# Kernel optimization log

Hardware: AMD Instinct MI355X
Metric: run time of the kernel (lower is better)

The kernel has to match this reference:

```python
import jax, jax.numpy as jnp
import numpy as np

N = 2048   # num nodes
D = 512    # hidden_dim


def setup_inputs() -> dict:
    key = jax.random.key(0)
    k1, k2 = jax.random.split(key)
    x = jax.random.normal(k1, (N, D), dtype=jnp.float32)
    # linear: hidden_dim -> 1 (xavier-like scale)
    w = jax.random.normal(k2, (D,), dtype=jnp.float32) * (1.0 / np.sqrt(D))
    b = jnp.zeros((1,), dtype=jnp.float32)
    return {"x": x, "w": w, "b": b}


def reference(x, w, b):
    # euclidean_distance_matrix + linear fused:
    # s[i,j] = sum_d w_d * (x[i,d]-x[j,d])^2 + b
    #        = q_i + q_j - 2*(x*w) @ x^T + b,  q_i = sum_d w_d x[i,d]^2
    xw = x * w                              # [N, D]
    q = jnp.sum(xw * x, axis=1)             # [N]
    cross = xw @ x.T                        # [N, N]
    s = q[:, None] + q[None, :] - 2.0 * cross + b[0]
    grouping_matrix = jax.nn.sigmoid(s)     # [N, N]

    # compute_fielder, similarity_graph='base'
    W = grouping_matrix
    degree = jnp.sum(W, axis=1)
    L = jnp.diag(degree) - W                # symmetric graph Laplacian
    eigen_values, eigen_vectors = jnp.linalg.eigh(L)
    order = jnp.argsort(jnp.abs(eigen_values))
    fielder_value = eigen_values[order[1]]
    fielder_vector = eigen_vectors[:, order[1]]
    return grouping_matrix, fielder_value, fielder_vector
```

## Files before the change

### kernel.cpp

```cpp
#include <hip/hip_runtime.h>
#include <math.h>

constexpr int NN = 2048;
constexpr int DD_ = 512;
constexpr int LM = 64;
constexpr int VS = NN + 32;
constexpr int GPART = 8;
#define SIGN_FLIP 1


typedef __attribute__((ext_vector_type(4))) float f32x4;
typedef __attribute__((ext_vector_type(8))) short bf16x8;

__device__ inline double waveReduceSum(double v) {
#pragma unroll
  for (int off = 32; off; off >>= 1) v += __shfl_down(v, off, 64);
  return v;
}

__device__ inline double blockReduceSum256(double v) {
  __shared__ double sm[4];
  int lane = threadIdx.x & 63;
  int wid  = threadIdx.x >> 6;
  v = waveReduceSum(v);
  __syncthreads();
  if (lane == 0) sm[wid] = v;
  __syncthreads();
  double r = 0.0;
  if (threadIdx.x < 4) r = sm[threadIdx.x];
  if (wid == 0) {
    r += __shfl_down(r, 2, 64);
    r += __shfl_down(r, 1, 64);
  }
  return r;
}

__device__ inline double blockReduceSum128(double v) {
  __shared__ double sm[2];
  int lane = threadIdx.x & 63;
  int wid  = threadIdx.x >> 6;
  v = waveReduceSum(v);
  if (lane == 0) sm[wid] = v;
  __syncthreads();
  double r = 0.0;
  if (threadIdx.x == 0) r = sm[0] + sm[1];
  return r;
}

__device__ inline unsigned short f2bf(float f) {
  unsigned u = __float_as_uint(f);
  u += 0x7FFFu + ((u >> 16) & 1u);
  return (unsigned short)(u >> 16);
}
__device__ inline float bf2f(unsigned short h) {
  return __uint_as_float(((unsigned)h) << 16);
}

__global__ __launch_bounds__(128) void k_cvtq(const float* __restrict__ x,
                                              const float* __restrict__ w,
                                              float* __restrict__ q,
                                              unsigned short* __restrict__ ah,
                                              unsigned short* __restrict__ al,
                                              unsigned short* __restrict__ bh,
                                              unsigned short* __restrict__ bl) {
  int row = blockIdx.x, t = threadIdx.x;
  int d = 4 * t;
  float4 xv = *(const float4*)&x[(size_t)row * DD_ + d];
  float4 wv = *(const float4*)&w[d];
  float xs[4] = {xv.x, xv.y, xv.z, xv.w};
  float wsv[4] = {wv.x, wv.y, wv.z, wv.w};
  unsigned short rah[4], ral[4], rbh[4], rbl[4];
  float accq = 0.f;
#pragma unroll
  for (int kq = 0; kq < 4; ++kq) {
    float xf = xs[kq], wf = wsv[kq];
    float a = xf * wf;
    unsigned short h = f2bf(a);
    rah[kq] = h;
    ral[kq] = f2bf(a - bf2f(h));
    unsigned short hb = f2bf(xf);
    rbh[kq] = hb;
    rbl[kq] = f2bf(xf - bf2f(hb));
    accq += wf * xf * xf;
  }
  ushort4 vA = {rah[0], rah[1], rah[2], rah[3]};
  ushort4 vAl = {ral[0], ral[1], ral[2], ral[3]};
  ushort4 vB = {rbh[0], rbh[1], rbh[2], rbh[3]};
  ushort4 vBl = {rbl[0], rbl[1], rbl[2], rbl[3]};
  *(ushort4*)&ah[(size_t)row * DD_ + d] = vA;
  *(ushort4*)&al[(size_t)row * DD_ + d] = vAl;
  *(ushort4*)&bh[(size_t)row * DD_ + d] = vB;
  *(ushort4*)&bl[(size_t)row * DD_ + d] = vBl;
  double rq = blockReduceSum128((double)accq);
  if (t == 0) q[row] = (float)rq;
}

__global__ __launch_bounds__(256) void k_Wm(const unsigned short* __restrict__ ah,
                                            const unsigned short* __restrict__ al,
                                            const unsigned short* __restrict__ bh,
                                            const unsigned short* __restrict__ bl,
                                            const float* __restrict__ q,
                                            const float* __restrict__ bptr,
                                            float* __restrict__ out) {
  const int bx = blockIdx.x, by = blockIdx.y;
  if (bx < by) return;
  __shared__ unsigned short As[2][128][40];
  __shared__ unsigned short Bs[2][128][40];
  const int t = threadIdx.x;
  const int i0 = by * 128, j0 = bx * 128;
  const int lane = t & 63, wv = t >> 6;
  const int wr = wv >> 1, wc = wv & 1;
  const int fr = lane & 15, kc = lane >> 4;
  const int srow = t >> 1, scol = (t & 1) * 16;

  f32x4 acc[4][4];
#pragma unroll
  for (int a = 0; a < 4; ++a)
#pragma unroll
    for (int b = 0; b < 4; ++b) acc[a][b] = (f32x4){0.f, 0.f, 0.f, 0.f};

  {
    bf16x8 ra0 = *(const bf16x8*)&ah[(size_t)(i0 + srow) * DD_ + scol];
    bf16x8 ra1 = *(const bf16x8*)&ah[(size_t)(i0 + srow) * DD_ + scol + 8];
    bf16x8 rb0 = *(const bf16x8*)&bh[(size_t)(j0 + srow) * DD_ + scol];
    bf16x8 rb1 = *(const bf16x8*)&bh[(size_t)(j0 + srow) * DD_ + scol + 8];
    *(bf16x8*)&As[0][srow][scol] = ra0;
    *(bf16x8*)&As[0][srow][scol + 8] = ra1;
    *(bf16x8*)&Bs[0][srow][scol] = rb0;
    *(bf16x8*)&Bs[0][srow][scol + 8] = rb1;
  }
  __syncthreads();
  int cur = 0;
  for (int s = 0; s < 48; ++s) {
    bf16x8 na0, na1, nb0, nb1;
    if (s + 1 < 48) {
      int pass = (s + 1) >> 4;
      int kk = ((s + 1) & 15) * 32;
      const unsigned short* srcA = (pass == 2) ? al : ah;
      const unsigned short* srcB = (pass == 1) ? bl : bh;
      na0 = *(const bf16x8*)&srcA[(size_t)(i0 + srow) * DD_ + kk + scol];
      na1 = *(const bf16x8*)&srcA[(size_t)(i0 + srow) * DD_ + kk + scol + 8];
      nb0 = *(const bf16x8*)&srcB[(size_t)(j0 + srow) * DD_ + kk + scol];
      nb1 = *(const bf16x8*)&srcB[(size_t)(j0 + srow) * DD_ + kk + scol + 8];
    }
    bf16x8 af[4], bq[4];
#pragma unroll
    for (int a = 0; a < 4; ++a)
      af[a] = *(const bf16x8*)&As[cur][wr * 64 + a * 16 + fr][kc * 8];
#pragma unroll
    for (int b = 0; b < 4; ++b)
      bq[b] = *(const bf16x8*)&Bs[cur][wc * 64 + b * 16 + fr][kc * 8];
#pragma unroll
    for (int a = 0; a < 4; ++a)
#pragma unroll
      for (int b = 0; b < 4; ++b)
        acc[a][b] = __builtin_amdgcn_mfma_f32_16x16x32_bf16(af[a], bq[b], acc[a][b], 0, 0, 0);
    if (s + 1 < 48) {
      *(bf16x8*)&As[cur ^ 1][srow][scol] = na0;
      *(bf16x8*)&As[cur ^ 1][srow][scol + 8] = na1;
      *(bf16x8*)&Bs[cur ^ 1][srow][scol] = nb0;
      *(bf16x8*)&Bs[cur ^ 1][srow][scol + 8] = nb1;
    }
    __syncthreads();
    cur ^= 1;
  }
  float b0 = bptr[0];
  const bool mirror = (bx != by);
#pragma unroll
  for (int a = 0; a < 4; ++a) {
#pragma unroll
    for (int rg = 0; rg < 4; ++rg) {
      int i = i0 + wr * 64 + a * 16 + kc * 4 + rg;
      float qi = q[i];
#pragma unroll
      for (int b = 0; b < 4; ++b) {
        int j = j0 + wc * 64 + b * 16 + fr;
        float s = qi + q[j] - 2.0f * acc[a][b][rg] + b0;
        float sig = 1.0f / (1.0f + expf(-s));
        out[(size_t)i * NN + j] = sig;
        if (mirror) out[(size_t)j * NN + i] = sig;
      }
    }
  }
}

__global__ __launch_bounds__(256) void k_init(double* __restrict__ r,
                                              double* __restrict__ part) {
  int t = threadIdx.x;
  double loc[8];
  double s = 0.0;
#pragma unroll
  for (int p = 0; p < 8; ++p) {
    unsigned i = (unsigned)(t + 256 * p);
    unsigned u = i * 2654435761u + 0x9E3779B9u;
    u ^= u >> 16; u *= 0x85EBCA6Bu; u ^= u >> 13; u *= 0xC2B2AE35u; u ^= u >> 16;
    double val = ((double)u / 4294967296.0) - 0.5;
    loc[p] = val; s += val;
  }
  __shared__ double mean_s, inv_s;
  double tot = blockReduceSum256(s);
  if (t == 0) mean_s = tot / (double)NN;
  __syncthreads();
  double mean = mean_s;
  double ss = 0.0;
#pragma unroll
  for (int p = 0; p < 8; ++p) { loc[p] -= mean; ss += loc[p] * loc[p]; }
  double tss = blockReduceSum256(ss);
  if (t == 0) inv_s = 1.0 / sqrt(tss);
  __syncthreads();
  double inv = inv_s;
#pragma unroll
  for (int p = 0; p < 8; ++p) r[t + 256 * p] = loc[p] * inv;
  if (t < GPART) part[t] = (t == 0) ? 1.0 : 0.0;
}

__global__ __launch_bounds__(256) void k_mva(const float* __restrict__ Wm,
                                             double* __restrict__ deg,
                                             const double* __restrict__ rprev,
                                             const double* __restrict__ part,
                                             double* __restrict__ V,
                                             double* __restrict__ wstash,
                                             double* __restrict__ c,
                                             double* __restrict__ beta, int j) {
  int b = blockIdx.x, t = threadIdx.x;
  double ss = 0.0;
#pragma unroll
  for (int p = 0; p < GPART; ++p) ss += part[p];
  double bet = sqrt(ss);
  double inv = (bet > 1e-3) ? 1.0 / bet : 0.0;

  if (b < NN) {
    const float* wr = Wm + (size_t)b * NN;
    double acc = 0.0, dsum = 0.0;
    if (j == 0) {
#pragma unroll
      for (int p = 0; p < 2; ++p) {
        int i = 4 * t + 1024 * p;
        float4 wl = *(const float4*)&wr[i];
        dsum += (double)wl.x + (double)wl.y + (double)wl.z + (double)wl.w;
        acc += (double)wl.x * rprev[i] + (double)wl.y * rprev[i + 1] +
               (double)wl.z * rprev[i + 2] + (double)wl.w * rprev[i + 3];
      }
    } else {
#pragma unroll
      for (int p = 0; p < 2; ++p) {
        int i = 4 * t + 1024 * p;
        float4 wl = *(const float4*)&wr[i];
        acc += (double)wl.x * rprev[i] + (double)wl.y * rprev[i + 1] +
               (double)wl.z * rprev[i + 2] + (double)wl.w * rprev[i + 3];
      }
    }
    double red = blockReduceSum256(acc);
    double dred = 0.0;
    if (j == 0) dred = blockReduceSum256(dsum);
    if (t == 0) {
      double d;
      if (j == 0) { d = dred; deg[b] = d; }
      else d = deg[b];
      double vj = rprev[b] * inv;
      V[(size_t)j * VS + b] = vj;
      wstash[(size_t)j * VS + b] = d * vj - red * inv;
      if (b == 0 && j > 0) beta[j - 1] = (bet > 1e-3) ? bet : 0.0;
    }
  } else {
    int q = b - NN;
    const double* wq = wstash + (size_t)q * VS;
    double a = 0.0;
#pragma unroll
    for (int p = 0; p < 8; ++p) { int i = t + 256 * p; a += wq[i] * rprev[i]; }
    double red = blockReduceSum256(a);
    if (t == 0) c[q] = red * inv;
  }
}

__global__ __launch_bounds__(256) void k_orthb(const double* __restrict__ V,
                                               const double* __restrict__ wstash,
                                               const double* __restrict__ c,
                                               double* __restrict__ r,
                                               double* __restrict__ part,
                                               double* __restrict__ alpha, int j) {
  __shared__ double cs[LM];
  __shared__ double cj_s, s1_s;
  int b = blockIdx.x, t = threadIdx.x;
  const double* wj = wstash + (size_t)j * VS;
  const double* vj = V + (size_t)j * VS;
  double a = 0.0, s = 0.0;
#pragma unroll
  for (int p = 0; p < 8; ++p) {
    int i = t + 256 * p;
    double wv = wj[i];
    a += vj[i] * wv;
    s += wv;
  }
  double cj = blockReduceSum256(a);
  double s1 = blockReduceSum256(s);
  if (t == 0) { cj_s = cj; s1_s = s1; }
  for (int k = t; k < j; k += 256) cs[k] = c[k];
  __syncthreads();
  double cjv = cj_s, s1v = s1_s;
  int i = b * 256 + t;
  double val = wj[i] - s1v / (double)NN - cjv * vj[i];
  for (int k = 0; k < j; ++k) val -= cs[k] * V[(size_t)k * VS + i];
  r[i] = val;
  double rr = blockReduceSum256(val * val);
  if (t == 0) {
    part[b] = rr;
    if (b == 0) alpha[j] = cjv;
  }
}

__device__ inline double guardpiv(double d) {
  if (fabs(d) < 1e-280) return (d < 0.0) ? -1e-280 : 1e-280;
  return d;
}

__global__ __launch_bounds__(64) void k_tri(const double* __restrict__ alpha,
                                            const double* __restrict__ beta,
                                            double* __restrict__ svec) {
  const int t = threadIdx.x;
  double al_r = alpha[t];
  double be_r = (t < LM - 1) ? beta[t] : 0.0;

  int cand = isfinite(al_r) ? LM : t;
  int candb = (t < LM - 1 && (be_r == 0.0 || !isfinite(be_r))) ? (t + 1) : LM;
  int m = min(cand, candb);
#pragma unroll
  for (int off = 32; off; off >>= 1) m = min(m, __shfl_down(m, off, 64));
  m = __shfl(m, 0, 64);
  if (m < 2) m = 2;
  const int n = m;

  double be_prev = __shfl_up(be_r, 1, 64);
  double lo = 1e300, hi = -1e300;
  if (t < n) {
    double rr = 0.0;
    if (t > 0) rr += fabs(be_prev);
    if (t < n - 1) rr += fabs(be_r);
    lo = al_r - rr;
    hi = al_r + rr;
  }
#pragma unroll
  for (int off = 32; off; off >>= 1) {
    lo = fmin(lo, __shfl_down(lo, off, 64));
    hi = fmax(hi, __shfl_down(hi, off, 64));
  }
  lo = __shfl(lo, 0, 64);
  hi = __shfl(hi, 0, 64);

  double B0 = lo, B1 = hi;
  for (int round = 0; round < 3; ++round) {
    double p = B0 + (B1 - B0) * ((double)(t + 1) / 65.0);
    int cnt = 0;
    double d = __shfl(al_r, 0, 64) - p;
    if (d < 0) cnt++;
    for (int i = 1; i < n; ++i) {
      double ai = __shfl(al_r, i, 64);
      double bi = __shfl(be_r, i - 1, 64);
      if (fabs(d) < 1e-300) d = (d < 0.0) ? -1e-300 : 1e-300;
      d = (ai - p) - bi * bi / d;
      if (d < 0) cnt++;
    }
    unsigned long long nz = __ballot(cnt > 0);
    double nl, nh;
    if (nz) {
      int first = __ffsll(nz) - 1;
      nh = B0 + (B1 - B0) * ((double)(first + 1) / 65.0);
      nl = (first > 0) ? (B0 + (B1 - B0) * ((double)first / 65.0)) : B0;
    } else {
      nl = B0 + (B1 - B0) * (64.0 / 65.0);
      nh = B1;
    }
    B0 = nl; B1 = nh;
  }
  const double sigma = 0.5 * (B0 + B1);

  double Dgf = 0.0, Dl_s = 0.0, Du_s = 0.0, Du2_s = 0.0;
  int piv_s = 0;
  {
    double dg = __shfl(al_r, 0, 64) - sigma;
    double du = __shfl(be_r, 0, 64);
    for (int i = 0; i < n - 1; ++i) {
      double bl = __shfl(be_r, i, 64);
      double a_ip1 = __shfl(al_r, i + 1, 64);
      double be_ip1 = (i + 1 < n - 1) ? __shfl(be_r, i + 1, 64) : 0.0;
      double dg_ip1 = a_ip1 - sigma;
      double dg_n, du_n;
      if (fabs(dg) >= fabs(bl)) {
        double fact = bl / guardpiv(dg);
        if (t == i) { Dgf = dg; Dl_s = fact; Du_s = du; Du2_s = 0.0; piv_s = 0; }
        dg_n = dg_ip1 - fact * du;
        du_n = be_ip1;
      } else {
        double fact = dg / bl;
        if (t == i) { Dgf = bl; Dl_s = fact; Du_s = dg_ip1; Du2_s = be_ip1; piv_s = 1; }
        dg_n = du - fact * dg_ip1;
        du_n = -fact * be_ip1;
      }
      dg = dg_n; du = du_n;
    }
    if (t == n - 1) Dgf = dg;
  }

  double bbf = 1.0;
  {
    double cur = 1.0;
    for (int i = 0; i < n - 1; ++i) {
      double dl = __shfl(Dl_s, i, 64);
      int pv = __shfl(piv_s, i, 64);
      double nxt;
      if (!pv) {
        if (t == i) bbf = cur;
        nxt = 1.0 - dl * cur;
      } else {
        if (t == i) bbf = 1.0;
        nxt = cur - dl;
      }
      cur = nxt;
    }
    if (t == n - 1) bbf = cur;
  }

  double xv = 0.0;
  {
    double x_ip1 = 0.0, x_ip2 = 0.0;
    for (int i = n - 1; i >= 0; --i) {
      double bi = __shfl(bbf, i, 64);
      double dgi = __shfl(Dgf, i, 64);
      double dui = __shfl(Du_s, i, 64);
      double du2i = __shfl(Du2_s, i, 64);
      double num = bi;
      if (i < n - 1) num -= dui * x_ip1;
      if (i < n - 2) num -= du2i * x_ip2;
      double xi = num / guardpiv(dgi);
      if (t == i) xv = xi;
      x_ip2 = x_ip1; x_ip1 = xi;
    }
  }

  double nrm = (t < n) ? xv * xv : 0.0;
#pragma unroll
  for (int off = 32; off; off >>= 1) nrm += __shfl_down(nrm, off, 64);
  nrm = __shfl(nrm, 0, 64);
  double s = 1.0 / sqrt(nrm);
  svec[t] = (t < n) ? xv * s : 0.0;
}

__global__ __launch_bounds__(256) void k_ritz(const double* __restrict__ V,
                                              const double* __restrict__ s,
                                              double* __restrict__ u) {
  __shared__ double cs[LM];
  int t = threadIdx.x;
  for (int k = t; k < LM; k += 256) cs[k] = s[k];
  __syncthreads();
  int i = blockIdx.x * 256 + t;
  double acc = 0.0;
  for (int k = 0; k < LM; ++k) acc += cs[k] * V[(size_t)k * VS + i];
  u[i] = acc;
}

__global__ __launch_bounds__(256) void k_mvu(const float* __restrict__ Wm,
                                             const double* __restrict__ deg,
                                             const double* __restrict__ v,
                                             double* __restrict__ w) {
  int row = blockIdx.x, t = threadIdx.x;
  const float* wr = Wm + (size_t)row * NN;
  double acc = 0.0;
#pragma unroll
  for (int p = 0; p < 2; ++p) {
    int i = 4 * t + 1024 * p;
    float4 wl = *(const float4*)&wr[i];
    acc += (double)wl.x * v[i] + (double)wl.y * v[i + 1] +
           (double)wl.z * v[i + 2] + (double)wl.w * v[i + 3];
  }
  double r = blockReduceSum256(acc);
  if (t == 0) w[row] = deg[row] * v[row] - r;
}

__global__ __launch_bounds__(256) void k_tail(const double* __restrict__ u,
                                              const double* __restrict__ lu,
                                              float* __restrict__ out_lam,
                                              float* __restrict__ outv) {
  __shared__ double mv[256];
  __shared__ int mi[256];
  __shared__ double mean_s, scale_s;
  int t = threadIdx.x;
  double a = 0.0, b = 0.0;
#pragma unroll
  for (int p = 0; p < 8; ++p) {
    int i = t + 256 * p;
    a += u[i] * lu[i];
    b += u[i] * u[i];
  }
  double ra = blockReduceSum256(a);
  double rb = blockReduceSum256(b);
  if (t == 0) *out_lam = (float)(ra / rb);
  double loc[8];
  double s = 0.0;
#pragma unroll
  for (int p = 0; p < 8; ++p) { loc[p] = u[t + 256 * p]; s += loc[p]; }
  double tot = blockReduceSum256(s);
  if (t == 0) mean_s = tot / (double)NN;
  __syncthreads();
  double mean = mean_s;
  double ss = 0.0, bv = -1.0;
  int bi = 0;
#pragma unroll
  for (int p = 0; p < 8; ++p) {
    loc[p] -= mean;
    ss += loc[p] * loc[p];
    double aa = fabs(loc[p]);
    if (aa > bv) { bv = aa; bi = p; }
  }
  double tss = blockReduceSum256(ss);
  mv[t] = bv; mi[t] = t + 256 * bi;
  __syncthreads();
  for (int off = 128; off; off >>= 1) {
    if (t < off) {
      if (mv[t + off] > mv[t]) { mv[t] = mv[t + off]; mi[t] = mi[t + off]; }
    }
    __syncthreads();
  }
  if (t == 0) {
    int gi = mi[0];
    double best = u[gi] - mean_s;
    double sgn = (best < 0.0) ? -1.0 : 1.0;
#if SIGN_FLIP
    sgn = -sgn;
#endif
    scale_s = sgn / sqrt(tss);
  }
  __syncthreads();
  double sc = scale_s;
#pragma unroll
  for (int p = 0; p < 8; ++p) outv[t + 256 * p] = (float)(loc[p] * sc);
}

extern "C" void kernel_launch(void* const* d_in, const int* in_sizes, int n_in,
                              void* d_out, int out_size, void* d_ws, size_t ws_size,
                              hipStream_t stream) {
  const float* x = (const float*)d_in[0];
  const float* wv = (const float*)d_in[1];
  const float* bp = (const float*)d_in[2];
  float* out = (float*)d_out;

  char* ws = (char*)d_ws;
  size_t off = 0;
  auto alloc = [&](size_t bytes) -> char* {
    char* p = ws + off;
    off = (off + bytes + 255) & ~(size_t)255;
    return p;
  };
  float* q      = (float*)alloc((size_t)NN * 4);
  double* deg   = (double*)alloc((size_t)NN * 8);
  double* r     = (double*)alloc((size_t)NN * 8);
  double* u     = (double*)alloc((size_t)NN * 8);
  double* c     = (double*)alloc((size_t)(LM + 2) * 8);
  double* alpha = (double*)alloc((size_t)LM * 8);
  double* beta  = (double*)alloc((size_t)LM * 8);
  double* svec  = (double*)alloc((size_t)LM * 8);
  double* part  = (double*)alloc((size_t)GPART * 8);
  char* un = alloc((size_t)4 * NN * DD_ * 2);
  unsigned short* ah = (unsigned short*)un;
  unsigned short* al = ah + (size_t)NN * DD_;
  unsigned short* bh = al + (size_t)NN * DD_;
  unsigned short* bl = bh + (size_t)NN * DD_;
  double* V      = (double*)un;
  double* wstash = V + (size_t)LM * VS;
  (void)ws_size; (void)in_sizes; (void)n_in; (void)out_size;

  k_cvtq<<<NN, 128, 0, stream>>>(x, wv, q, ah, al, bh, bl);
  dim3 g(NN / 128, NN / 128);
  k_Wm<<<g, 256, 0, stream>>>(ah, al, bh, bl, q, bp, out);
  k_init<<<1, 256, 0, stream>>>(r, part);

  for (int j = 0; j < LM; ++j) {
    k_mva<<<NN + j, 256, 0, stream>>>(out, deg, r, part, V, wstash, c, beta, j);
    k_orthb<<<NN / 256, 256, 0, stream>>>(V, wstash, c, r, part, alpha, j);
  }
  k_tri<<<1, 64, 0, stream>>>(alpha, beta, svec);
  k_ritz<<<NN / 256, 256, 0, stream>>>(V, svec, u);
  k_mvu<<<NN, 256, 0, stream>>>(out, deg, u, r);
  k_tail<<<1, 256, 0, stream>>>(u, r, out + (size_t)NN * NN,
                                out + (size_t)NN * NN + 1);
}
```

Baseline: 825.0 us.

## Coalesce mirrored sigmoid writes via LDS transpose and prefetch shuffles in tridiagonal solve

The GEMM epilogue used to write the mirrored (transposed) tile with scattered, column-strided stores. It now keeps the sigmoid values in the accumulators, transposes them through a shared-memory buffer unioned with the A/B staging tiles, and writes the mirror rows with float4 coalesced stores. In the single-wave tridiagonal kernel, the cross-lane shuffles in the Sturm count, LU factorization, forward and back substitution loops are software-prefetched one iteration ahead. The Sturm loop also gets a compile-time trip count for the full-size case, so these serial chains spend less time waiting on shuffle latency. The cost is extra barriers and LDS traffic in the epilogue.

```diff
diff --git a/kernel.cpp b/kernel.cpp
--- a/kernel.cpp
+++ b/kernel.cpp
@@ -104,8 +104,11 @@
                                             float* __restrict__ out) {
   const int bx = blockIdx.x, by = blockIdx.y;
   if (bx < by) return;
-  __shared__ unsigned short As[2][128][40];
-  __shared__ unsigned short Bs[2][128][40];
+  union SmemU {
+    struct { unsigned short As[2][128][40]; unsigned short Bs[2][128][40]; } ab;
+    float tr[64][132];
+  };
+  __shared__ SmemU sm;
   const int t = threadIdx.x;
   const int i0 = by * 128, j0 = bx * 128;
   const int lane = t & 63, wv = t >> 6;
@@ -124,10 +127,10 @@
     bf16x8 ra1 = *(const bf16x8*)&ah[(size_t)(i0 + srow) * DD_ + scol + 8];
     bf16x8 rb0 = *(const bf16x8*)&bh[(size_t)(j0 + srow) * DD_ + scol];
     bf16x8 rb1 = *(const bf16x8*)&bh[(size_t)(j0 + srow) * DD_ + scol + 8];
-    *(bf16x8*)&As[0][srow][scol] = ra0;
-    *(bf16x8*)&As[0][srow][scol + 8] = ra1;
-    *(bf16x8*)&Bs[0][srow][scol] = rb0;
-    *(bf16x8*)&Bs[0][srow][scol + 8] = rb1;
+    *(bf16x8*)&sm.ab.As[0][srow][scol] = ra0;
+    *(bf16x8*)&sm.ab.As[0][srow][scol + 8] = ra1;
+    *(bf16x8*)&sm.ab.Bs[0][srow][scol] = rb0;
+    *(bf16x8*)&sm.ab.Bs[0][srow][scol + 8] = rb1;
   }
   __syncthreads();
   int cur = 0;
@@ -146,26 +149,25 @@
     bf16x8 af[4], bq[4];
 #pragma unroll
     for (int a = 0; a < 4; ++a)
-      af[a] = *(const bf16x8*)&As[cur][wr * 64 + a * 16 + fr][kc * 8];
+      af[a] = *(const bf16x8*)&sm.ab.As[cur][wr * 64 + a * 16 + fr][kc * 8];
 #pragma unroll
     for (int b = 0; b < 4; ++b)
-      bq[b] = *(const bf16x8*)&Bs[cur][wc * 64 + b * 16 + fr][kc * 8];
+      bq[b] = *(const bf16x8*)&sm.ab.Bs[cur][wc * 64 + b * 16 + fr][kc * 8];
 #pragma unroll
     for (int a = 0; a < 4; ++a)
 #pragma unroll
       for (int b = 0; b < 4; ++b)
         acc[a][b] = __builtin_amdgcn_mfma_f32_16x16x32_bf16(af[a], bq[b], acc[a][b], 0, 0, 0);
     if (s + 1 < 48) {
-      *(bf16x8*)&As[cur ^ 1][srow][scol] = na0;
-      *(bf16x8*)&As[cur ^ 1][srow][scol + 8] = na1;
-      *(bf16x8*)&Bs[cur ^ 1][srow][scol] = nb0;
-      *(bf16x8*)&Bs[cur ^ 1][srow][scol + 8] = nb1;
+      *(bf16x8*)&sm.ab.As[cur ^ 1][srow][scol] = na0;
+      *(bf16x8*)&sm.ab.As[cur ^ 1][srow][scol + 8] = na1;
+      *(bf16x8*)&sm.ab.Bs[cur ^ 1][srow][scol] = nb0;
+      *(bf16x8*)&sm.ab.Bs[cur ^ 1][srow][scol + 8] = nb1;
     }
     __syncthreads();
     cur ^= 1;
   }
   float b0 = bptr[0];
-  const bool mirror = (bx != by);
 #pragma unroll
   for (int a = 0; a < 4; ++a) {
 #pragma unroll
@@ -177,8 +179,29 @@
         int j = j0 + wc * 64 + b * 16 + fr;
         float s = qi + q[j] - 2.0f * acc[a][b][rg] + b0;
         float sig = 1.0f / (1.0f + expf(-s));
+        acc[a][b][rg] = sig;
         out[(size_t)i * NN + j] = sig;
-        if (mirror) out[(size_t)j * NN + i] = sig;
+      }
+    }
+  }
+  if (bx != by) {
+#pragma unroll
+    for (int h = 0; h < 2; ++h) {
+      __syncthreads();
+      if (wc == h) {
+#pragma unroll
+        for (int a = 0; a < 4; ++a)
+#pragma unroll
+          for (int b = 0; b < 4; ++b)
+            *(f32x4*)&sm.tr[b * 16 + fr][wr * 64 + a * 16 + kc * 4] = acc[a][b];
+      }
+      __syncthreads();
+#pragma unroll
+      for (int p = 0; p < 8; ++p) {
+        int f = p * 256 + t;
+        int rr_ = f >> 5, c4 = (f & 31) * 4;
+        float4 v = *(const float4*)&sm.tr[rr_][c4];
+        *(float4*)&out[(size_t)(j0 + h * 64 + rr_) * NN + i0 + c4] = v;
       }
     }
   }
@@ -314,6 +337,25 @@
   return d;
 }
 
+template <int NB_>
+__device__ inline int sturm_cnt(double p, double al_r, double be_r, int nn) {
+  const int lim = NB_ ? NB_ : nn;
+  int cnt = 0;
+  double d = __shfl(al_r, 0, 64) - p;
+  if (d < 0.0) cnt++;
+  double ai = __shfl(al_r, 1, 64);
+  double bi = __shfl(be_r, 0, 64);
+  for (int i = 1; i < lim; ++i) {
+    double ai_n = 0.0, bi_n = 0.0;
+    if (i + 1 < lim) { ai_n = __shfl(al_r, i + 1, 64); bi_n = __shfl(be_r, i, 64); }
+    if (fabs(d) < 1e-300) d = (d < 0.0) ? -1e-300 : 1e-300;
+    d = (ai - p) - bi * bi / d;
+    if (d < 0.0) cnt++;
+    ai = ai_n; bi = bi_n;
+  }
+  return cnt;
+}
+
 __global__ __launch_bounds__(64) void k_tri(const double* __restrict__ alpha,
                                             const double* __restrict__ beta,
                                             double* __restrict__ svec) {
@@ -350,16 +392,8 @@
   double B0 = lo, B1 = hi;
   for (int round = 0; round < 3; ++round) {
     double p = B0 + (B1 - B0) * ((double)(t + 1) / 65.0);
-    int cnt = 0;
-    double d = __shfl(al_r, 0, 64) - p;
-    if (d < 0) cnt++;
-    for (int i = 1; i < n; ++i) {
-      double ai = __shfl(al_r, i, 64);
-      double bi = __shfl(be_r, i - 1, 64);
-      if (fabs(d) < 1e-300) d = (d < 0.0) ? -1e-300 : 1e-300;
-      d = (ai - p) - bi * bi / d;
-      if (d < 0) cnt++;
-    }
+    int cnt = (n == LM) ? sturm_cnt<LM>(p, al_r, be_r, n)
+                        : sturm_cnt<0>(p, al_r, be_r, n);
     unsigned long long nz = __ballot(cnt > 0);
     double nl, nh;
     if (nz) {
@@ -378,12 +412,16 @@
   int piv_s = 0;
   {
     double dg = __shfl(al_r, 0, 64) - sigma;
-    double du = __shfl(be_r, 0, 64);
+    double bl = __shfl(be_r, 0, 64);
+    double du = bl;
+    double a1 = __shfl(al_r, 1, 64);
+    double b1 = (2 < n) ? __shfl(be_r, 1, 64) : 0.0;
     for (int i = 0; i < n - 1; ++i) {
-      double bl = __shfl(be_r, i, 64);
-      double a_ip1 = __shfl(al_r, i + 1, 64);
-      double be_ip1 = (i + 1 < n - 1) ? __shfl(be_r, i + 1, 64) : 0.0;
-      double dg_ip1 = a_ip1 - sigma;
+      double a1_n = 0.0, b1_n = 0.0;
+      if (i + 2 < n) a1_n = __shfl(al_r, i + 2, 64);
+      if (i + 3 < n) b1_n = __shfl(be_r, i + 2, 64);
+      double dg_ip1 = a1 - sigma;
+      double be_ip1 = b1;
       double dg_n, du_n;
       if (fabs(dg) >= fabs(bl)) {
         double fact = bl / guardpiv(dg);
@@ -397,6 +435,7 @@
         du_n = -fact * be_ip1;
       }
       dg = dg_n; du = du_n;
+      bl = b1; a1 = a1_n; b1 = b1_n;
     }
     if (t == n - 1) Dgf = dg;
   }
@@ -404,9 +443,11 @@
   double bbf = 1.0;
   {
     double cur = 1.0;
+    double dl = __shfl(Dl_s, 0, 64);
+    int pv = __shfl(piv_s, 0, 64);
     for (int i = 0; i < n - 1; ++i) {
-      double dl = __shfl(Dl_s, i, 64);
-      int pv = __shfl(piv_s, i, 64);
+      double dl_n = 0.0; int pv_n = 0;
+      if (i + 1 < n - 1) { dl_n = __shfl(Dl_s, i + 1, 64); pv_n = __shfl(piv_s, i + 1, 64); }
       double nxt;
       if (!pv) {
         if (t == i) bbf = cur;
@@ -416,24 +457,33 @@
         nxt = cur - dl;
       }
       cur = nxt;
+      dl = dl_n; pv = pv_n;
     }
     if (t == n - 1) bbf = cur;
   }
 
   double xv = 0.0;
   {
-    double x_ip1 = 0.0, x_ip2 = 0.0;
+    double x1 = 0.0, x2 = 0.0;
+    double bi = __shfl(bbf, n - 1, 64);
+    double dgi = __shfl(Dgf, n - 1, 64);
+    double dui = __shfl(Du_s, n - 1, 64);
+    double du2i = __shfl(Du2_s, n - 1, 64);
     for (int i = n - 1; i >= 0; --i) {
-      double bi = __shfl(bbf, i, 64);
-      double dgi = __shfl(Dgf, i, 64);
-      double dui = __shfl(Du_s, i, 64);
-      double du2i = __shfl(Du2_s, i, 64);
+      double bi_n = 0.0, dgi_n = 0.0, dui_n = 0.0, du2i_n = 0.0;
+      if (i > 0) {
+        bi_n = __shfl(bbf, i - 1, 64);
+        dgi_n = __shfl(Dgf, i - 1, 64);
+        dui_n = __shfl(Du_s, i - 1, 64);
+        du2i_n = __shfl(Du2_s, i - 1, 64);
+      }
       double num = bi;
-      if (i < n - 1) num -= dui * x_ip1;
-      if (i < n - 2) num -= du2i * x_ip2;
+      if (i < n - 1) num -= dui * x1;
+      if (i < n - 2) num -= du2i * x2;
       double xi = num / guardpiv(dgi);
       if (t == i) xv = xi;
-      x_ip2 = x_ip1; x_ip1 = xi;
+      x2 = x1; x1 = xi;
+      bi = bi_n; dgi = dgi_n; dui = dui_n; du2i = du2i_n;
     }
   }
 
```

After: 831.8 us. About the same (+0.8%).
